# Optimization experiments

Measured on AMD Instinct MI355X. Metric: run time of the kernel, lower is better.

The kernel has to match this reference:

```python
import jax, jax.numpy as jnp
import numpy as np

# Model dims
B, S, H, E, I, K = 2, 2048, 1024, 8, 1024, 2
ALPHA, LIMIT = 1.702, 7.0  # gpt_oss activation constants (module defaults)


def setup_inputs() -> dict:
    key = jax.random.key(0)
    ks = jax.random.split(key, 5)
    sc = 0.02
    return {
        "hidden_states": jax.random.normal(ks[0], (B, S, H), jnp.float32),
        "router_weight": jax.random.normal(ks[1], (H, E), jnp.float32) * sc,
        "gate_up_proj": jax.random.normal(ks[2], (E, H, 2 * I), jnp.float32) * sc,
        "gate_up_proj_bias": jnp.zeros((E, 2 * I), jnp.float32),
        "down_proj": jax.random.normal(ks[3], (E, I, H), jnp.float32) * sc,
        "down_proj_bias": jnp.zeros((E, H), jnp.float32),
    }


def reference(hidden_states, router_weight, gate_up_proj, gate_up_proj_bias,
              down_proj, down_proj_bias):
    Bt, St, Ht = hidden_states.shape
    x = hidden_states.reshape(-1, Ht)           # [T, H], T = B*S
    T = x.shape[0]

    # Router: linear -> top-k -> softmax over selected logits (gpt_oss style)
    logits = x @ router_weight                  # [T, E]
    top_vals, top_idx = jax.lax.top_k(logits, K)
    scores = jax.nn.softmax(top_vals, axis=-1)  # [T, K]
    # Sparse combine weights: w[t, e] = score if e selected for t, else 0
    w = jnp.zeros((T, E), x.dtype).at[jnp.arange(T)[:, None], top_idx].set(scores)

    # Fused gate+up projection for every expert (dense equivalent of grouped GEMM;
    # unselected experts get zero combine weight so math matches sparse path)
    gu = jnp.einsum('th,ehf->tef', x, gate_up_proj) + gate_up_proj_bias  # [T, E, 2I]
    gate = gu[..., ::2]                         # interleaved gate (default)
    up = gu[..., 1::2]
    gate = jnp.minimum(gate, LIMIT)
    up = jnp.clip(up, -LIMIT, LIMIT)
    glu = gate * jax.nn.sigmoid(gate * ALPHA)
    act = (up + 1.0) * glu                      # [T, E, I]

    down = jnp.einsum('tei,eih->teh', act, down_proj) + down_proj_bias  # [T, E, H]

    # Weighted combine over experts (all-to-all combine is identity at D=1)
    out = jnp.einsum('te,teh->th', w, down)     # [T, H]
    return out.reshape(Bt, St, Ht)
```

## Files before the change

### kernel.cpp

```cpp
#include <hip/hip_runtime.h>
#include <hip/hip_bf16.h>
#include <cstdint>
#include <cstddef>

constexpr int T_TOK = 4096;
constexpr int H_DIM = 1024;
constexpr int E_NUM = 8;
constexpr int I_DIM = 1024;
constexpr int F2    = 2048;
constexpr float ALPHA = 1.702f;
constexpr float LIMIT = 7.0f;
constexpr int BM = 128;
constexpr int BK = 64;
constexpr int NKT = 16;
constexpr int MAXT = 72;

using u16    = unsigned short;
using bf16x8 = __attribute__((ext_vector_type(8))) __bf16;
using s16x8  = __attribute__((ext_vector_type(8))) short;
using f32x4  = __attribute__((ext_vector_type(4))) float;

constexpr size_t WS_W1T  = 0;
constexpr size_t WS_DOWN = 0;
constexpr size_t WS_W2T  = 33554432;
constexpr size_t WS_ACT  = 50331648;
constexpr size_t WS_ETOK = 67108864;
constexpr size_t WS_POS  = 67239936;
constexpr size_t WS_CNT  = 67272704;
constexpr size_t WS_ROWB = 67272736;
constexpr size_t WS_ASGN = 67272768;
constexpr size_t WS_TOPE = 67273792;
constexpr size_t WS_TOPW = 67290176;
constexpr size_t WS_XBF  = 67322944;
constexpr size_t WS_NEED = 75711552;

__device__ __forceinline__ u16 f2bf(float f) {
    union { float f; unsigned u; } v; v.f = f;
    return (u16)((v.u + 0x7FFFu + ((v.u >> 16) & 1u)) >> 16);
}
__device__ __forceinline__ float bf2f(u16 u) {
    union { unsigned u; float f; } v; v.u = (unsigned)u << 16; return v.f;
}

__device__ __forceinline__ s16x8 pack8(float4 a, float4 b) {
    s16x8 r;
    r[0] = (short)f2bf(a.x); r[1] = (short)f2bf(a.y);
    r[2] = (short)f2bf(a.z); r[3] = (short)f2bf(a.w);
    r[4] = (short)f2bf(b.x); r[5] = (short)f2bf(b.y);
    r[6] = (short)f2bf(b.z); r[7] = (short)f2bf(b.w);
    return r;
}

__device__ __forceinline__ void gload16(const void* g, void* l) {
    __builtin_amdgcn_global_load_lds((const __attribute__((address_space(1))) unsigned*)g,
                                     (__attribute__((address_space(3))) unsigned*)l,
                                     16, 0, 0);
}

__device__ __forceinline__ void pipe_sync() {
    __builtin_amdgcn_sched_barrier(0);
    asm volatile("s_waitcnt vmcnt(0) lgkmcnt(0)" ::: "memory");
    __builtin_amdgcn_s_barrier();
    __builtin_amdgcn_sched_barrier(0);
}

__global__ __launch_bounds__(256) void k_xbf(const float* __restrict__ x,
                                             u16* __restrict__ xbf) {
    const size_t i = ((size_t)blockIdx.x * 256 + threadIdx.x) * 8;
    float4 a = *(const float4*)(x + i);
    float4 b = *(const float4*)(x + i + 4);
    *(s16x8*)(xbf + i) = pack8(a, b);
}

__global__ __launch_bounds__(256) void k_transpose_w1(const float* __restrict__ in,
                                                      u16* __restrict__ out) {
    __shared__ float tile[64][65];
    const int e = blockIdx.z, c0 = blockIdx.x * 64, h0 = blockIdx.y * 64;
    const int tid = threadIdx.x;
    const float* src = in + ((size_t)e * H_DIM + h0) * F2 + c0;
#pragma unroll
    for (int i = 0; i < 4; ++i) {
        int r = (tid >> 4) + i * 16, c = (tid & 15) * 4;
        float4 v = *(const float4*)(src + (size_t)r * F2 + c);
        tile[r][c] = v.x; tile[r][c + 1] = v.y; tile[r][c + 2] = v.z; tile[r][c + 3] = v.w;
    }
    __syncthreads();
    const int c = tid >> 2, hseg = (tid & 3) * 16;
    const int g = c & 1;
    const int f = (c0 + c) >> 1;
    u16* dst = out + (((size_t)e * 2 + g) * I_DIM + f) * H_DIM + h0 + hseg;
    s16x8 o0, o1;
#pragma unroll
    for (int j = 0; j < 8; ++j) o0[j] = (short)f2bf(tile[hseg + j][c]);
#pragma unroll
    for (int j = 0; j < 8; ++j) o1[j] = (short)f2bf(tile[hseg + 8 + j][c]);
    *(s16x8*)dst = o0;
    *(s16x8*)(dst + 8) = o1;
}

__global__ __launch_bounds__(256) void k_transpose_w2(const float* __restrict__ in,
                                                      u16* __restrict__ out) {
    __shared__ float tile[64][65];
    const int e = blockIdx.z, h0 = blockIdx.x * 64, i0 = blockIdx.y * 64;
    const int tid = threadIdx.x;
    const float* src = in + ((size_t)e * I_DIM + i0) * H_DIM + h0;
#pragma unroll
    for (int i = 0; i < 4; ++i) {
        int r = (tid >> 4) + i * 16, c = (tid & 15) * 4;
        float4 v = *(const float4*)(src + (size_t)r * H_DIM + c);
        tile[r][c] = v.x; tile[r][c + 1] = v.y; tile[r][c + 2] = v.z; tile[r][c + 3] = v.w;
    }
    __syncthreads();
    const int c = tid >> 2, iseg = (tid & 3) * 16;
    u16* dst = out + ((size_t)e * H_DIM + h0 + c) * I_DIM + i0 + iseg;
    s16x8 o0, o1;
#pragma unroll
    for (int j = 0; j < 8; ++j) o0[j] = (short)f2bf(tile[iseg + j][c]);
#pragma unroll
    for (int j = 0; j < 8; ++j) o1[j] = (short)f2bf(tile[iseg + 8 + j][c]);
    *(s16x8*)dst = o0;
    *(s16x8*)(dst + 8) = o1;
}

__global__ __launch_bounds__(256) void k_router_top2(const float* __restrict__ x,
                                                     const float* __restrict__ rw,
                                                     int* __restrict__ tope,
                                                     float2* __restrict__ topw) {
    const int wave = threadIdx.x >> 6, lane = threadIdx.x & 63;
    const int t = blockIdx.x * 4 + wave;
    const float* xr = x + (size_t)t * H_DIM;
    float acc[E_NUM];
#pragma unroll
    for (int e = 0; e < E_NUM; ++e) acc[e] = 0.f;
    for (int h = lane; h < H_DIM; h += 64) {
        float xv = xr[h];
        const float* r = rw + h * E_NUM;
#pragma unroll
        for (int e = 0; e < E_NUM; ++e) acc[e] += xv * r[e];
    }
#pragma unroll
    for (int e = 0; e < E_NUM; ++e) {
        float v = acc[e];
#pragma unroll
        for (int o = 32; o > 0; o >>= 1) v += __shfl_down(v, o);
        acc[e] = v;
    }
    if (lane == 0) {
        int e0 = 0; float v0 = acc[0];
#pragma unroll
        for (int e = 1; e < E_NUM; ++e) if (acc[e] > v0) { v0 = acc[e]; e0 = e; }
        int e1 = -1; float v1 = -3.4e38f;
#pragma unroll
        for (int e = 0; e < E_NUM; ++e) if (e != e0 && acc[e] > v1) { v1 = acc[e]; e1 = e; }
        float ew = expf(v1 - v0);
        float inv = 1.f / (1.f + ew);
        tope[t] = e0 | (e1 << 8);
        topw[t] = make_float2(inv, ew * inv);
    }
}

__global__ __launch_bounds__(256) void k_router_scatter(const int* __restrict__ tope,
                                                        int* __restrict__ cnt,
                                                        int* __restrict__ ent_tok,
                                                        int2* __restrict__ pos) {
    __shared__ int lcnt[E_NUM];
    __shared__ int gbase[E_NUM];
    const int tid = threadIdx.x;
    const int t = blockIdx.x * 256 + tid;
    if (tid < E_NUM) lcnt[tid] = 0;
    __syncthreads();
    const int pk = tope[t];
    const int e0 = pk & 0xff, e1 = pk >> 8;
    const int o0 = atomicAdd(&lcnt[e0], 1);
    const int o1 = atomicAdd(&lcnt[e1], 1);
    __syncthreads();
    if (tid < E_NUM) gbase[tid] = atomicAdd(&cnt[tid], lcnt[tid]);
    __syncthreads();
    const int p0 = gbase[e0] + o0;
    const int p1 = gbase[e1] + o1;
    ent_tok[e0 * T_TOK + p0] = t;
    ent_tok[e1 * T_TOK + p1] = t;
    pos[t] = make_int2(p0, p1);
}

__global__ void k_schedule(const int* __restrict__ cnt, int* __restrict__ rowbase,
                           int* __restrict__ assign) {
    if (threadIdx.x == 0) {
        int rb = 0, na = 0;
        for (int e = 0; e < E_NUM; ++e) {
            rowbase[e] = rb;
            int nt = (cnt[e] + BM - 1) >> 7;
            for (int m = 0; m < nt; ++m) assign[na++] = (e << 16) | m;
            rb += cnt[e];
        }
        for (; na < MAXT; ++na) assign[na] = -1;
    }
}

__global__ __launch_bounds__(256, 2) void k_gemm1(
    const u16* __restrict__ xbf, const u16* __restrict__ w1t,
    const float* __restrict__ bias, const int* __restrict__ ent_tok,
    const int* __restrict__ cnt, const int* __restrict__ rowbase,
    const int* __restrict__ assign, u16* __restrict__ act) {
    const int a = assign[blockIdx.y];
    if (a < 0) return;
    const int e = a >> 16, mt = a & 0xffff;
    const int j0 = blockIdx.x * 64;
    const int cs = cnt[e], r0 = mt * BM;
    __shared__ __align__(16) u16 As[2][BM * BK];
    __shared__ __align__(16) u16 Bs[2][BM * BK];
    const int tid = threadIdx.x, lane = tid & 63, wv = tid >> 6;
    const int lr8 = lane >> 3;
    const int sg  = (lane & 7) ^ lr8;
    const u16* asrc[4]; const u16* bsrc[4]; int dofs[4];
#pragma unroll
    for (int j = 0; j < 4; ++j) {
        const int row = j * 32 + wv * 8 + lr8;
        const int aent = r0 + row;
        const int tok = (aent < cs) ? ent_tok[e * T_TOK + aent] : 0;
        asrc[j] = xbf + (size_t)tok * H_DIM + sg * 8;
        const int g = row >> 6;
        const int f = j0 + (row & 63);
        bsrc[j] = w1t + (((size_t)e * 2 + g) * I_DIM + f) * H_DIM + sg * 8;
        dofs[j] = (j * 32 + wv * 8) * BK;
    }
    const int wm = wv >> 1, wn = wv & 1;
    const int lcol = lane & 15, lk = lane >> 4;
    int aoff[4][2], goff[2][2], uoff[2][2];
#pragma unroll
    for (int mi = 0; mi < 4; ++mi) {
        const int r = wm * 64 + mi * 16 + lcol;
#pragma unroll
        for (int h = 0; h < 2; ++h)
            aoff[mi][h] = r * 128 + (((h * 4 + lk) ^ (r & 7)) << 4);
    }
#pragma unroll
    for (int nj = 0; nj < 2; ++nj) {
        const int rg_ = wn * 32 + nj * 16 + lcol;
        const int ru  = 64 + rg_;
#pragma unroll
        for (int h = 0; h < 2; ++h) {
            goff[nj][h] = rg_ * 128 + (((h * 4 + lk) ^ (rg_ & 7)) << 4);
            uoff[nj][h] = ru  * 128 + (((h * 4 + lk) ^ (ru  & 7)) << 4);
        }
    }
    f32x4 ag[4][2], au[4][2];
    const f32x4 z = {0.f, 0.f, 0.f, 0.f};
#pragma unroll
    for (int mi = 0; mi < 4; ++mi) { ag[mi][0] = z; ag[mi][1] = z; au[mi][0] = z; au[mi][1] = z; }
#pragma unroll
    for (int j = 0; j < 4; ++j) {
        gload16(asrc[j], &As[0][dofs[j]]);
        gload16(bsrc[j], &Bs[0][dofs[j]]);
    }
    pipe_sync();
    int cur = 0;
    for (int t = 0; t < NKT; ++t) {
        if (t + 1 < NKT) {
            const int kn = (t + 1) * BK;
            u16* Ad = As[cur ^ 1]; u16* Bd = Bs[cur ^ 1];
#pragma unroll
            for (int j = 0; j < 4; ++j) {
                gload16(asrc[j] + kn, Ad + dofs[j]);
                gload16(bsrc[j] + kn, Bd + dofs[j]);
            }
        }
        const char* Ab = (const char*)(&As[cur][0]);
        const char* Bb = (const char*)(&Bs[cur][0]);
#pragma unroll
        for (int h = 0; h < 2; ++h) {
            bf16x8 af[4];
#pragma unroll
            for (int mi = 0; mi < 4; ++mi) af[mi] = *(const bf16x8*)(Ab + aoff[mi][h]);
            const bf16x8 g0 = *(const bf16x8*)(Bb + goff[0][h]);
            const bf16x8 g1 = *(const bf16x8*)(Bb + goff[1][h]);
            const bf16x8 u0 = *(const bf16x8*)(Bb + uoff[0][h]);
            const bf16x8 u1 = *(const bf16x8*)(Bb + uoff[1][h]);
            __builtin_amdgcn_s_setprio(1);
#pragma unroll
            for (int mi = 0; mi < 4; ++mi) {
                ag[mi][0] = __builtin_amdgcn_mfma_f32_16x16x32_bf16(af[mi], g0, ag[mi][0], 0, 0, 0);
                au[mi][0] = __builtin_amdgcn_mfma_f32_16x16x32_bf16(af[mi], u0, au[mi][0], 0, 0, 0);
                ag[mi][1] = __builtin_amdgcn_mfma_f32_16x16x32_bf16(af[mi], g1, ag[mi][1], 0, 0, 0);
                au[mi][1] = __builtin_amdgcn_mfma_f32_16x16x32_bf16(af[mi], u1, au[mi][1], 0, 0, 0);
            }
            __builtin_amdgcn_s_setprio(0);
        }
        pipe_sync();
        cur ^= 1;
    }
    const int rbase = rowbase[e];
#pragma unroll
    for (int mi = 0; mi < 4; ++mi) {
#pragma unroll
        for (int nj = 0; nj < 2; ++nj) {
            const int col = j0 + wn * 32 + nj * 16 + lcol;
            const float bg_ = bias[e * F2 + 2 * col];
            const float bu_ = bias[e * F2 + 2 * col + 1];
#pragma unroll
            for (int rg = 0; rg < 4; ++rg) {
                const int r = wm * 64 + mi * 16 + lk * 4 + rg;
                if (r0 + r < cs) {
                    float gv = ag[mi][nj][rg] + bg_;
                    float uv = au[mi][nj][rg] + bu_;
                    gv = fminf(gv, LIMIT);
                    uv = fminf(fmaxf(uv, -LIMIT), LIMIT);
                    const float glu = gv / (1.f + expf(-ALPHA * gv));
                    act[(size_t)(rbase + r0 + r) * I_DIM + col] = f2bf((uv + 1.f) * glu);
                }
            }
        }
    }
}

__global__ __launch_bounds__(256, 2) void k_gemm2(
    const u16* __restrict__ act, const u16* __restrict__ w2t,
    const int* __restrict__ cnt, const int* __restrict__ rowbase,
    const int* __restrict__ assign, u16* __restrict__ down) {
    const int a = assign[blockIdx.y];
    if (a < 0) return;
    const int e = a >> 16, mt = a & 0xffff;
    const int n0 = blockIdx.x * 128;
    const int cs = cnt[e], r0 = mt * BM, rbase = rowbase[e];
    __shared__ __align__(16) u16 As[2][BM * BK];
    __shared__ __align__(16) u16 Bs[2][BM * BK];
    const int tid = threadIdx.x, lane = tid & 63, wv = tid >> 6;
    const int lr8 = lane >> 3;
    const int sg  = (lane & 7) ^ lr8;
    const u16* asrc[4]; const u16* bsrc[4]; int dofs[4];
#pragma unroll
    for (int j = 0; j < 4; ++j) {
        const int row = j * 32 + wv * 8 + lr8;
        int ar = rbase + r0 + row;
        if (ar > 2 * T_TOK - 1) ar = 2 * T_TOK - 1;
        asrc[j] = act + (size_t)ar * I_DIM + sg * 8;
        bsrc[j] = w2t + ((size_t)e * H_DIM + n0 + row) * I_DIM + sg * 8;
        dofs[j] = (j * 32 + wv * 8) * BK;
    }
    const int wm = wv >> 1, wn = wv & 1;
    const int lcol = lane & 15, lk = lane >> 4;
    int aoff[4][2], boff[4][2];
#pragma unroll
    for (int mi = 0; mi < 4; ++mi) {
        const int r = wm * 64 + mi * 16 + lcol;
        const int b = wn * 64 + mi * 16 + lcol;
#pragma unroll
        for (int h = 0; h < 2; ++h) {
            aoff[mi][h] = r * 128 + (((h * 4 + lk) ^ (r & 7)) << 4);
            boff[mi][h] = b * 128 + (((h * 4 + lk) ^ (b & 7)) << 4);
        }
    }
    f32x4 acc[4][4];
    const f32x4 z = {0.f, 0.f, 0.f, 0.f};
#pragma unroll
    for (int mi = 0; mi < 4; ++mi)
#pragma unroll
        for (int nj = 0; nj < 4; ++nj) acc[mi][nj] = z;
#pragma unroll
    for (int j = 0; j < 4; ++j) {
        gload16(asrc[j], &As[0][dofs[j]]);
        gload16(bsrc[j], &Bs[0][dofs[j]]);
    }
    pipe_sync();
    int cur = 0;
    for (int t = 0; t < NKT; ++t) {
        if (t + 1 < NKT) {
            const int kn = (t + 1) * BK;
            u16* Ad = As[cur ^ 1]; u16* Bd = Bs[cur ^ 1];
#pragma unroll
            for (int j = 0; j < 4; ++j) {
                gload16(asrc[j] + kn, Ad + dofs[j]);
                gload16(bsrc[j] + kn, Bd + dofs[j]);
            }
        }
        const char* Ab = (const char*)(&As[cur][0]);
        const char* Bb = (const char*)(&Bs[cur][0]);
#pragma unroll
        for (int h = 0; h < 2; ++h) {
            bf16x8 af[4], bf_[4];
#pragma unroll
            for (int mi = 0; mi < 4; ++mi) af[mi]  = *(const bf16x8*)(Ab + aoff[mi][h]);
#pragma unroll
            for (int nj = 0; nj < 4; ++nj) bf_[nj] = *(const bf16x8*)(Bb + boff[nj][h]);
            __builtin_amdgcn_s_setprio(1);
#pragma unroll
            for (int mi = 0; mi < 4; ++mi)
#pragma unroll
                for (int nj = 0; nj < 4; ++nj)
                    acc[mi][nj] = __builtin_amdgcn_mfma_f32_16x16x32_bf16(af[mi], bf_[nj], acc[mi][nj], 0, 0, 0);
            __builtin_amdgcn_s_setprio(0);
        }
        pipe_sync();
        cur ^= 1;
    }
#pragma unroll
    for (int mi = 0; mi < 4; ++mi) {
#pragma unroll
        for (int nj = 0; nj < 4; ++nj) {
            const int col = n0 + wn * 64 + nj * 16 + lcol;
#pragma unroll
            for (int rg = 0; rg < 4; ++rg) {
                const int r = wm * 64 + mi * 16 + lk * 4 + rg;
                if (r0 + r < cs)
                    down[(size_t)(rbase + r0 + r) * H_DIM + col] = f2bf(acc[mi][nj][rg]);
            }
        }
    }
}

__global__ __launch_bounds__(256) void k_combine(
    const int* __restrict__ tope, const float2* __restrict__ topw,
    const int2* __restrict__ pos, const int* __restrict__ rowb,
    const float* __restrict__ b2, const u16* __restrict__ down,
    float* __restrict__ out) {
    const int t = blockIdx.x;
    const int c = threadIdx.x * 4;
    const int pk = tope[t];
    const int e0 = pk & 0xff, e1 = pk >> 8;
    const int2 pp = pos[t];
    const float2 w = topw[t];
    const size_t ro0 = (size_t)(rowb[e0] + pp.x) * H_DIM;
    const size_t ro1 = (size_t)(rowb[e1] + pp.y) * H_DIM;
    ushort4 d0 = *(const ushort4*)(down + ro0 + c);
    ushort4 d1 = *(const ushort4*)(down + ro1 + c);
    float4 bb0 = *(const float4*)(b2 + e0 * H_DIM + c);
    float4 bb1 = *(const float4*)(b2 + e1 * H_DIM + c);
    float4 o;
    o.x = w.x * (bf2f(d0.x) + bb0.x) + w.y * (bf2f(d1.x) + bb1.x);
    o.y = w.x * (bf2f(d0.y) + bb0.y) + w.y * (bf2f(d1.y) + bb1.y);
    o.z = w.x * (bf2f(d0.z) + bb0.z) + w.y * (bf2f(d1.z) + bb1.z);
    o.w = w.x * (bf2f(d0.w) + bb0.w) + w.y * (bf2f(d1.w) + bb1.w);
    *(float4*)(out + (size_t)t * H_DIM + c) = o;
}

extern "C" void kernel_launch(void* const* d_in, const int* in_sizes, int n_in,
                              void* d_out, int out_size, void* d_ws, size_t ws_size,
                              hipStream_t stream) {
    const float* x   = (const float*)d_in[0];
    const float* rw  = (const float*)d_in[1];
    const float* w1  = (const float*)d_in[2];
    const float* b1  = (const float*)d_in[3];
    const float* w2  = (const float*)d_in[4];
    const float* b2  = (const float*)d_in[5];
    float* out = (float*)d_out;
    char* ws = (char*)d_ws;

    if (ws_size < WS_NEED) return;

    u16*    W1T  = (u16*)(ws + WS_W1T);
    u16*    DOWN = (u16*)(ws + WS_DOWN);
    u16*    W2T  = (u16*)(ws + WS_W2T);
    u16*    ACT  = (u16*)(ws + WS_ACT);
    int*    ETOK = (int*)(ws + WS_ETOK);
    int2*   POS  = (int2*)(ws + WS_POS);
    int*    CNT  = (int*)(ws + WS_CNT);
    int*    ROWB = (int*)(ws + WS_ROWB);
    int*    ASGN = (int*)(ws + WS_ASGN);
    int*    TOPE = (int*)(ws + WS_TOPE);
    float2* TOPW = (float2*)(ws + WS_TOPW);
    u16*    XBF  = (u16*)(ws + WS_XBF);

    hipMemsetAsync(CNT, 0, E_NUM * sizeof(int), stream);

    k_xbf<<<T_TOK * H_DIM / 2048, 256, 0, stream>>>(x, XBF);
    k_transpose_w1<<<dim3(32, 16, 8), 256, 0, stream>>>(w1, W1T);
    k_transpose_w2<<<dim3(16, 16, 8), 256, 0, stream>>>(w2, W2T);
    k_router_top2<<<T_TOK / 4, 256, 0, stream>>>(x, rw, TOPE, TOPW);
    k_router_scatter<<<T_TOK / 256, 256, 0, stream>>>(TOPE, CNT, ETOK, POS);
    k_schedule<<<1, 64, 0, stream>>>(CNT, ROWB, ASGN);
    k_gemm1<<<dim3(16, MAXT), 256, 0, stream>>>(XBF, W1T, b1, ETOK, CNT, ROWB, ASGN, ACT);
    k_gemm2<<<dim3(8, MAXT), 256, 0, stream>>>(ACT, W2T, CNT, ROWB, ASGN, DOWN);
    k_combine<<<T_TOK, 256, 0, stream>>>(TOPE, TOPW, POS, ROWB, b2, DOWN, out);
}
```

Baseline: 179.4 us.

## Rework expert GEMMs into 512-thread blocks with quarter-staged pipelined loads

Both grouped GEMM kernels move to 8-wave blocks with larger tiles: gemm1 covers 128 tokens by 128 activation columns, and gemm2 covers 256 rows by 128 columns with its own tile schedule. The K loop is split into four sub-phases, each issuing part of the next tile's global-to-LDS loads with a partial vmcnt wait before its MFMAs, replacing the single full drain per tile. The aim is better overlap of memory and compute, more operand reuse per block and fewer blocks. The cost is more barriers per iteration, hand-tuned wait counts that must match the load order exactly, and a larger LDS footprint that may cut occupancy.

```diff
diff --git a/kernel.cpp b/kernel.cpp
--- a/kernel.cpp
+++ b/kernel.cpp
@@ -10,10 +10,10 @@
 constexpr int F2    = 2048;
 constexpr float ALPHA = 1.702f;
 constexpr float LIMIT = 7.0f;
-constexpr int BM = 128;
-constexpr int BK = 64;
+constexpr int BK  = 64;
 constexpr int NKT = 16;
-constexpr int MAXT = 72;
+constexpr int MAXT1 = 72;
+constexpr int MAXT2 = 40;
 
 using u16    = unsigned short;
 using bf16x8 = __attribute__((ext_vector_type(8))) __bf16;
@@ -28,7 +28,8 @@
 constexpr size_t WS_POS  = 67239936;
 constexpr size_t WS_CNT  = 67272704;
 constexpr size_t WS_ROWB = 67272736;
-constexpr size_t WS_ASGN = 67272768;
+constexpr size_t WS_ASG1 = 67272768;
+constexpr size_t WS_ASG2 = 67272768 + 512;
 constexpr size_t WS_TOPE = 67273792;
 constexpr size_t WS_TOPW = 67290176;
 constexpr size_t WS_XBF  = 67322944;
@@ -57,12 +58,8 @@
                                      16, 0, 0);
 }
 
-__device__ __forceinline__ void pipe_sync() {
-    __builtin_amdgcn_sched_barrier(0);
-    asm volatile("s_waitcnt vmcnt(0) lgkmcnt(0)" ::: "memory");
-    __builtin_amdgcn_s_barrier();
-    __builtin_amdgcn_sched_barrier(0);
-}
+#define BAR() __builtin_amdgcn_s_barrier()
+#define WVM(n) asm volatile("s_waitcnt vmcnt(" #n ")" ::: "memory")
 
 __global__ __launch_bounds__(256) void k_xbf(const float* __restrict__ x,
                                              u16* __restrict__ xbf) {
@@ -184,20 +181,23 @@
 }
 
 __global__ void k_schedule(const int* __restrict__ cnt, int* __restrict__ rowbase,
-                           int* __restrict__ assign) {
+                           int* __restrict__ a1, int* __restrict__ a2) {
     if (threadIdx.x == 0) {
-        int rb = 0, na = 0;
+        int rb = 0, n1 = 0, n2 = 0;
         for (int e = 0; e < E_NUM; ++e) {
             rowbase[e] = rb;
-            int nt = (cnt[e] + BM - 1) >> 7;
-            for (int m = 0; m < nt; ++m) assign[na++] = (e << 16) | m;
+            int t1 = (cnt[e] + 127) >> 7;
+            for (int m = 0; m < t1; ++m) a1[n1++] = (e << 16) | m;
+            int t2 = (cnt[e] + 255) >> 8;
+            for (int m = 0; m < t2; ++m) a2[n2++] = (e << 16) | m;
             rb += cnt[e];
         }
-        for (; na < MAXT; ++na) assign[na] = -1;
-    }
-}
-
-__global__ __launch_bounds__(256, 2) void k_gemm1(
+        for (; n1 < MAXT1; ++n1) a1[n1] = -1;
+        for (; n2 < MAXT2; ++n2) a2[n2] = -1;
+    }
+}
+
+__global__ __launch_bounds__(512, 2) void k_gemm1(
     const u16* __restrict__ xbf, const u16* __restrict__ w1t,
     const float* __restrict__ bias, const int* __restrict__ ent_tok,
     const int* __restrict__ cnt, const int* __restrict__ rowbase,
@@ -205,207 +205,348 @@
     const int a = assign[blockIdx.y];
     if (a < 0) return;
     const int e = a >> 16, mt = a & 0xffff;
-    const int j0 = blockIdx.x * 64;
-    const int cs = cnt[e], r0 = mt * BM;
-    __shared__ __align__(16) u16 As[2][BM * BK];
-    __shared__ __align__(16) u16 Bs[2][BM * BK];
+    const int j0 = blockIdx.x * 128;
+    const int cs = cnt[e], r0 = mt * 128, rbase = rowbase[e];
+    __shared__ __align__(16) u16 As[2 * 2 * 64 * 64];
+    __shared__ __align__(16) u16 Bs[2 * 2 * 128 * 64];
     const int tid = threadIdx.x, lane = tid & 63, wv = tid >> 6;
+    const int lcol = lane & 15, lk = lane >> 4;
     const int lr8 = lane >> 3;
-    const int sg  = (lane & 7) ^ lr8;
-    const u16* asrc[4]; const u16* bsrc[4]; int dofs[4];
-#pragma unroll
-    for (int j = 0; j < 4; ++j) {
-        const int row = j * 32 + wv * 8 + lr8;
-        const int aent = r0 + row;
-        const int tok = (aent < cs) ? ent_tok[e * T_TOK + aent] : 0;
-        asrc[j] = xbf + (size_t)tok * H_DIM + sg * 8;
-        const int g = row >> 6;
-        const int f = j0 + (row & 63);
-        bsrc[j] = w1t + (((size_t)e * 2 + g) * I_DIM + f) * H_DIM + sg * 8;
-        dofs[j] = (j * 32 + wv * 8) * BK;
-    }
-    const int wm = wv >> 1, wn = wv & 1;
-    const int lcol = lane & 15, lk = lane >> 4;
-    int aoff[4][2], goff[2][2], uoff[2][2];
-#pragma unroll
-    for (int mi = 0; mi < 4; ++mi) {
-        const int r = wm * 64 + mi * 16 + lcol;
-#pragma unroll
-        for (int h = 0; h < 2; ++h)
-            aoff[mi][h] = r * 128 + (((h * 4 + lk) ^ (r & 7)) << 4);
-    }
-#pragma unroll
-    for (int nj = 0; nj < 2; ++nj) {
-        const int rg_ = wn * 32 + nj * 16 + lcol;
-        const int ru  = 64 + rg_;
-#pragma unroll
-        for (int h = 0; h < 2; ++h) {
-            goff[nj][h] = rg_ * 128 + (((h * 4 + lk) ^ (rg_ & 7)) << 4);
-            uoff[nj][h] = ru  * 128 + (((h * 4 + lk) ^ (ru  & 7)) << 4);
+    const int sg  = (lane & 7) ^ (lr8 & 7);
+
+    const int arow0 = 0 * 64 + wv * 8 + lr8;
+    const int arow1 = 1 * 64 + wv * 8 + lr8;
+    const int ae0 = r0 + arow0, ae1 = r0 + arow1;
+    const int tok0 = (ae0 < cs) ? ent_tok[e * T_TOK + ae0] : 0;
+    const int tok1 = (ae1 < cs) ? ent_tok[e * T_TOK + ae1] : 0;
+    const u16* aS0 = xbf + (size_t)tok0 * H_DIM + sg * 8;
+    const u16* aS1 = xbf + (size_t)tok1 * H_DIM + sg * 8;
+    const u16* bS[2][2];
+#pragma unroll
+    for (int h = 0; h < 2; ++h)
+#pragma unroll
+        for (int i = 0; i < 2; ++i) {
+            const int brow = h * 128 + i * 64 + wv * 8 + lr8;
+            const int pair = brow >> 4, gu = pair & 1;
+            const int acol = j0 + (pair >> 1) * 16 + (brow & 15);
+            bS[h][i] = w1t + (((size_t)e * 2 + gu) * I_DIM + acol) * H_DIM + sg * 8;
         }
-    }
-    f32x4 ag[4][2], au[4][2];
+
+    int swz[2];
+#pragma unroll
+    for (int kk = 0; kk < 2; ++kk) swz[kk] = (((kk * 4 + lk) ^ (lcol & 7)) << 4);
+    int aro[2], bro[2];
+#pragma unroll
+    for (int mi = 0; mi < 2; ++mi) aro[mi] = ((wv & 1) * 32 + mi * 16 + lcol) * 128;
+#pragma unroll
+    for (int nj = 0; nj < 2; ++nj) bro[nj] = ((wv >> 1) * 32 + nj * 16 + lcol) * 128;
+    const char* AbC = (const char*)As;
+    const char* BbC = (const char*)Bs;
+
+    f32x4 acc[2][2][2][2];
     const f32x4 z = {0.f, 0.f, 0.f, 0.f};
 #pragma unroll
-    for (int mi = 0; mi < 4; ++mi) { ag[mi][0] = z; ag[mi][1] = z; au[mi][0] = z; au[mi][1] = z; }
-#pragma unroll
-    for (int j = 0; j < 4; ++j) {
-        gload16(asrc[j], &As[0][dofs[j]]);
-        gload16(bsrc[j], &Bs[0][dofs[j]]);
-    }
-    pipe_sync();
-    int cur = 0;
-    for (int t = 0; t < NKT; ++t) {
-        if (t + 1 < NKT) {
-            const int kn = (t + 1) * BK;
-            u16* Ad = As[cur ^ 1]; u16* Bd = Bs[cur ^ 1];
-#pragma unroll
-            for (int j = 0; j < 4; ++j) {
-                gload16(asrc[j] + kn, Ad + dofs[j]);
-                gload16(bsrc[j] + kn, Bd + dofs[j]);
-            }
-        }
-        const char* Ab = (const char*)(&As[cur][0]);
-        const char* Bb = (const char*)(&Bs[cur][0]);
-#pragma unroll
-        for (int h = 0; h < 2; ++h) {
-            bf16x8 af[4];
-#pragma unroll
-            for (int mi = 0; mi < 4; ++mi) af[mi] = *(const bf16x8*)(Ab + aoff[mi][h]);
-            const bf16x8 g0 = *(const bf16x8*)(Bb + goff[0][h]);
-            const bf16x8 g1 = *(const bf16x8*)(Bb + goff[1][h]);
-            const bf16x8 u0 = *(const bf16x8*)(Bb + uoff[0][h]);
-            const bf16x8 u1 = *(const bf16x8*)(Bb + uoff[1][h]);
-            __builtin_amdgcn_s_setprio(1);
-#pragma unroll
-            for (int mi = 0; mi < 4; ++mi) {
-                ag[mi][0] = __builtin_amdgcn_mfma_f32_16x16x32_bf16(af[mi], g0, ag[mi][0], 0, 0, 0);
-                au[mi][0] = __builtin_amdgcn_mfma_f32_16x16x32_bf16(af[mi], u0, au[mi][0], 0, 0, 0);
-                ag[mi][1] = __builtin_amdgcn_mfma_f32_16x16x32_bf16(af[mi], g1, ag[mi][1], 0, 0, 0);
-                au[mi][1] = __builtin_amdgcn_mfma_f32_16x16x32_bf16(af[mi], u1, au[mi][1], 0, 0, 0);
-            }
-            __builtin_amdgcn_s_setprio(0);
-        }
-        pipe_sync();
-        cur ^= 1;
-    }
-    const int rbase = rowbase[e];
-#pragma unroll
-    for (int mi = 0; mi < 4; ++mi) {
-#pragma unroll
-        for (int nj = 0; nj < 2; ++nj) {
-            const int col = j0 + wn * 32 + nj * 16 + lcol;
-            const float bg_ = bias[e * F2 + 2 * col];
-            const float bu_ = bias[e * F2 + 2 * col + 1];
-#pragma unroll
-            for (int rg = 0; rg < 4; ++rg) {
-                const int r = wm * 64 + mi * 16 + lk * 4 + rg;
-                if (r0 + r < cs) {
-                    float gv = ag[mi][nj][rg] + bg_;
-                    float uv = au[mi][nj][rg] + bu_;
-                    gv = fminf(gv, LIMIT);
-                    uv = fminf(fmaxf(uv, -LIMIT), LIMIT);
-                    const float glu = gv / (1.f + expf(-ALPHA * gv));
-                    act[(size_t)(rbase + r0 + r) * I_DIM + col] = f2bf((uv + 1.f) * glu);
+    for (int mh = 0; mh < 2; ++mh)
+#pragma unroll
+        for (int mi = 0; mi < 2; ++mi)
+#pragma unroll
+            for (int nh = 0; nh < 2; ++nh)
+#pragma unroll
+                for (int nj = 0; nj < 2; ++nj) acc[mh][mi][nh][nj] = z;
+
+    gload16(aS0, (u16*)As + 0 * 4096 + wv * 512);
+    gload16(aS1, (u16*)As + 1 * 4096 + wv * 512);
+    gload16(bS[0][0], (u16*)Bs + 0 * 8192 + 0 * 4096 + wv * 512);
+    gload16(bS[0][1], (u16*)Bs + 0 * 8192 + 1 * 4096 + wv * 512);
+    gload16(bS[1][0], (u16*)Bs + 1 * 8192 + 0 * 4096 + wv * 512);
+    gload16(bS[1][1], (u16*)Bs + 1 * 8192 + 1 * 4096 + wv * 512);
+    WVM(0);
+    BAR();
+
+    bf16x8 aF[2][2], bF0[2][2], bF1[2][2];
+
+    for (int kt = 0; kt < NKT; ++kt) {
+        const int d = kt & 1, d2 = d ^ 1;
+        const int dA = d * 16384, dB = d * 32768;
+        const int kno = (kt + 1) * BK;
+        const bool st = (kt + 1 < NKT);
+
+        if (st) { gload16(aS0 + kno, (u16*)As + (d2 * 2 + 0) * 4096 + wv * 512); WVM(4); }
+        else    { WVM(3); }
+        BAR();
+#pragma unroll
+        for (int mi = 0; mi < 2; ++mi)
+#pragma unroll
+            for (int kk = 0; kk < 2; ++kk)
+                aF[mi][kk] = *(const bf16x8*)(AbC + dA + 0 * 8192 + aro[mi] + swz[kk]);
+#pragma unroll
+        for (int nj = 0; nj < 2; ++nj)
+#pragma unroll
+            for (int kk = 0; kk < 2; ++kk)
+                bF0[nj][kk] = *(const bf16x8*)(BbC + dB + 0 * 16384 + bro[nj] + swz[kk]);
+        __builtin_amdgcn_s_setprio(1);
+#pragma unroll
+        for (int mi = 0; mi < 2; ++mi)
+#pragma unroll
+            for (int nj = 0; nj < 2; ++nj)
+#pragma unroll
+                for (int kk = 0; kk < 2; ++kk)
+                    acc[0][mi][0][nj] = __builtin_amdgcn_mfma_f32_16x16x32_bf16(aF[mi][kk], bF0[nj][kk], acc[0][mi][0][nj], 0, 0, 0);
+        __builtin_amdgcn_s_setprio(0);
+        BAR();
+
+        if (st) {
+            gload16(bS[0][0] + kno, (u16*)Bs + (d2 * 2 + 0) * 8192 + 0 * 4096 + wv * 512);
+            gload16(bS[0][1] + kno, (u16*)Bs + (d2 * 2 + 0) * 8192 + 1 * 4096 + wv * 512);
+            WVM(4);
+        } else { WVM(1); }
+        BAR();
+#pragma unroll
+        for (int nj = 0; nj < 2; ++nj)
+#pragma unroll
+            for (int kk = 0; kk < 2; ++kk)
+                bF1[nj][kk] = *(const bf16x8*)(BbC + dB + 1 * 16384 + bro[nj] + swz[kk]);
+        __builtin_amdgcn_s_setprio(1);
+#pragma unroll
+        for (int mi = 0; mi < 2; ++mi)
+#pragma unroll
+            for (int nj = 0; nj < 2; ++nj)
+#pragma unroll
+                for (int kk = 0; kk < 2; ++kk)
+                    acc[0][mi][1][nj] = __builtin_amdgcn_mfma_f32_16x16x32_bf16(aF[mi][kk], bF1[nj][kk], acc[0][mi][1][nj], 0, 0, 0);
+        __builtin_amdgcn_s_setprio(0);
+        BAR();
+
+        if (st) {
+            gload16(bS[1][0] + kno, (u16*)Bs + (d2 * 2 + 1) * 8192 + 0 * 4096 + wv * 512);
+            gload16(bS[1][1] + kno, (u16*)Bs + (d2 * 2 + 1) * 8192 + 1 * 4096 + wv * 512);
+            WVM(5);
+        } else { WVM(0); }
+        BAR();
+#pragma unroll
+        for (int mi = 0; mi < 2; ++mi)
+#pragma unroll
+            for (int kk = 0; kk < 2; ++kk)
+                aF[mi][kk] = *(const bf16x8*)(AbC + dA + 1 * 8192 + aro[mi] + swz[kk]);
+        __builtin_amdgcn_s_setprio(1);
+#pragma unroll
+        for (int mi = 0; mi < 2; ++mi)
+#pragma unroll
+            for (int nj = 0; nj < 2; ++nj)
+#pragma unroll
+                for (int kk = 0; kk < 2; ++kk)
+                    acc[1][mi][0][nj] = __builtin_amdgcn_mfma_f32_16x16x32_bf16(aF[mi][kk], bF0[nj][kk], acc[1][mi][0][nj], 0, 0, 0);
+        __builtin_amdgcn_s_setprio(0);
+        BAR();
+
+        if (st) gload16(aS1 + kno, (u16*)As + (d2 * 2 + 1) * 4096 + wv * 512);
+        BAR();
+        __builtin_amdgcn_s_setprio(1);
+#pragma unroll
+        for (int mi = 0; mi < 2; ++mi)
+#pragma unroll
+            for (int nj = 0; nj < 2; ++nj)
+#pragma unroll
+                for (int kk = 0; kk < 2; ++kk)
+                    acc[1][mi][1][nj] = __builtin_amdgcn_mfma_f32_16x16x32_bf16(aF[mi][kk], bF1[nj][kk], acc[1][mi][1][nj], 0, 0, 0);
+        __builtin_amdgcn_s_setprio(0);
+        BAR();
+    }
+
+#pragma unroll
+    for (int mh = 0; mh < 2; ++mh)
+#pragma unroll
+        for (int mi = 0; mi < 2; ++mi)
+#pragma unroll
+            for (int nh = 0; nh < 2; ++nh) {
+                const int acol = j0 + (nh * 4 + (wv >> 1)) * 16 + lcol;
+                const float bg_ = bias[e * F2 + 2 * acol];
+                const float bu_ = bias[e * F2 + 2 * acol + 1];
+#pragma unroll
+                for (int rg = 0; rg < 4; ++rg) {
+                    const int row = mh * 64 + (wv & 1) * 32 + mi * 16 + lk * 4 + rg;
+                    if (r0 + row < cs) {
+                        float gv = acc[mh][mi][nh][0][rg] + bg_;
+                        float uv = acc[mh][mi][nh][1][rg] + bu_;
+                        gv = fminf(gv, LIMIT);
+                        uv = fminf(fmaxf(uv, -LIMIT), LIMIT);
+                        const float glu = gv / (1.f + expf(-ALPHA * gv));
+                        act[(size_t)(rbase + r0 + row) * I_DIM + acol] = f2bf((uv + 1.f) * glu);
+                    }
                 }
             }
-        }
-    }
-}
-
-__global__ __launch_bounds__(256, 2) void k_gemm2(
-    const u16* __restrict__ act, const u16* __restrict__ w2t,
+}
+
+__global__ __launch_bounds__(512, 2) void k_gemm2(
+    const u16* __restrict__ actb, const u16* __restrict__ w2t,
     const int* __restrict__ cnt, const int* __restrict__ rowbase,
     const int* __restrict__ assign, u16* __restrict__ down) {
     const int a = assign[blockIdx.y];
     if (a < 0) return;
     const int e = a >> 16, mt = a & 0xffff;
     const int n0 = blockIdx.x * 128;
-    const int cs = cnt[e], r0 = mt * BM, rbase = rowbase[e];
-    __shared__ __align__(16) u16 As[2][BM * BK];
-    __shared__ __align__(16) u16 Bs[2][BM * BK];
+    const int cs = cnt[e], r0 = mt * 256, rbase = rowbase[e];
+    __shared__ __align__(16) u16 As[2 * 2 * 128 * 64];
+    __shared__ __align__(16) u16 Bs[2 * 2 * 64 * 64];
     const int tid = threadIdx.x, lane = tid & 63, wv = tid >> 6;
+    const int lcol = lane & 15, lk = lane >> 4;
     const int lr8 = lane >> 3;
-    const int sg  = (lane & 7) ^ lr8;
-    const u16* asrc[4]; const u16* bsrc[4]; int dofs[4];
-#pragma unroll
-    for (int j = 0; j < 4; ++j) {
-        const int row = j * 32 + wv * 8 + lr8;
-        int ar = rbase + r0 + row;
-        if (ar > 2 * T_TOK - 1) ar = 2 * T_TOK - 1;
-        asrc[j] = act + (size_t)ar * I_DIM + sg * 8;
-        bsrc[j] = w2t + ((size_t)e * H_DIM + n0 + row) * I_DIM + sg * 8;
-        dofs[j] = (j * 32 + wv * 8) * BK;
-    }
-    const int wm = wv >> 1, wn = wv & 1;
-    const int lcol = lane & 15, lk = lane >> 4;
-    int aoff[4][2], boff[4][2];
-#pragma unroll
-    for (int mi = 0; mi < 4; ++mi) {
-        const int r = wm * 64 + mi * 16 + lcol;
-        const int b = wn * 64 + mi * 16 + lcol;
-#pragma unroll
-        for (int h = 0; h < 2; ++h) {
-            aoff[mi][h] = r * 128 + (((h * 4 + lk) ^ (r & 7)) << 4);
-            boff[mi][h] = b * 128 + (((h * 4 + lk) ^ (b & 7)) << 4);
+    const int sg  = (lane & 7) ^ (lr8 & 7);
+
+    const u16* aS[2][2];
+#pragma unroll
+    for (int h = 0; h < 2; ++h)
+#pragma unroll
+        for (int i = 0; i < 2; ++i) {
+            const int row = h * 128 + i * 64 + wv * 8 + lr8;
+            int ar = rbase + r0 + row;
+            if (ar > 2 * T_TOK - 1) ar = 2 * T_TOK - 1;
+            aS[h][i] = actb + (size_t)ar * I_DIM + sg * 8;
         }
-    }
-    f32x4 acc[4][4];
+    const u16* bS[2];
+#pragma unroll
+    for (int h = 0; h < 2; ++h) {
+        const int brow = h * 64 + wv * 8 + lr8;
+        bS[h] = w2t + ((size_t)e * H_DIM + n0 + brow) * I_DIM + sg * 8;
+    }
+
+    int swz[2];
+#pragma unroll
+    for (int kk = 0; kk < 2; ++kk) swz[kk] = (((kk * 4 + lk) ^ (lcol & 7)) << 4);
+    int aro[2], bro[2];
+#pragma unroll
+    for (int mi = 0; mi < 2; ++mi) aro[mi] = ((wv & 3) * 32 + mi * 16 + lcol) * 128;
+#pragma unroll
+    for (int nj = 0; nj < 2; ++nj) bro[nj] = ((wv >> 2) * 32 + nj * 16 + lcol) * 128;
+    const char* AbC = (const char*)As;
+    const char* BbC = (const char*)Bs;
+
+    f32x4 acc[2][2][2][2];
     const f32x4 z = {0.f, 0.f, 0.f, 0.f};
 #pragma unroll
-    for (int mi = 0; mi < 4; ++mi)
-#pragma unroll
-        for (int nj = 0; nj < 4; ++nj) acc[mi][nj] = z;
-#pragma unroll
-    for (int j = 0; j < 4; ++j) {
-        gload16(asrc[j], &As[0][dofs[j]]);
-        gload16(bsrc[j], &Bs[0][dofs[j]]);
-    }
-    pipe_sync();
-    int cur = 0;
-    for (int t = 0; t < NKT; ++t) {
-        if (t + 1 < NKT) {
-            const int kn = (t + 1) * BK;
-            u16* Ad = As[cur ^ 1]; u16* Bd = Bs[cur ^ 1];
-#pragma unroll
-            for (int j = 0; j < 4; ++j) {
-                gload16(asrc[j] + kn, Ad + dofs[j]);
-                gload16(bsrc[j] + kn, Bd + dofs[j]);
-            }
+    for (int mh = 0; mh < 2; ++mh)
+#pragma unroll
+        for (int mi = 0; mi < 2; ++mi)
+#pragma unroll
+            for (int nh = 0; nh < 2; ++nh)
+#pragma unroll
+                for (int nj = 0; nj < 2; ++nj) acc[mh][mi][nh][nj] = z;
+
+    gload16(aS[0][0], (u16*)As + 0 * 8192 + 0 * 4096 + wv * 512);
+    gload16(aS[0][1], (u16*)As + 0 * 8192 + 1 * 4096 + wv * 512);
+    gload16(bS[0],    (u16*)Bs + 0 * 4096 + wv * 512);
+    gload16(bS[1],    (u16*)Bs + 1 * 4096 + wv * 512);
+    gload16(aS[1][0], (u16*)As + 1 * 8192 + 0 * 4096 + wv * 512);
+    gload16(aS[1][1], (u16*)As + 1 * 8192 + 1 * 4096 + wv * 512);
+    WVM(0);
+    BAR();
+
+    bf16x8 aF[2][2], bF0[2][2], bF1[2][2];
+
+    for (int kt = 0; kt < NKT; ++kt) {
+        const int d = kt & 1, d2 = d ^ 1;
+        const int dA = d * 32768, dB = d * 16384;
+        const int kno = (kt + 1) * BK;
+        const bool st = (kt + 1 < NKT);
+
+        if (st) {
+            gload16(aS[0][0] + kno, (u16*)As + (d2 * 2 + 0) * 8192 + 0 * 4096 + wv * 512);
+            gload16(aS[0][1] + kno, (u16*)As + (d2 * 2 + 0) * 8192 + 1 * 4096 + wv * 512);
+            WVM(5);
+        } else { WVM(3); }
+        BAR();
+#pragma unroll
+        for (int mi = 0; mi < 2; ++mi)
+#pragma unroll
+            for (int kk = 0; kk < 2; ++kk)
+                aF[mi][kk] = *(const bf16x8*)(AbC + dA + 0 * 16384 + aro[mi] + swz[kk]);
+#pragma unroll
+        for (int nj = 0; nj < 2; ++nj)
+#pragma unroll
+            for (int kk = 0; kk < 2; ++kk)
+                bF0[nj][kk] = *(const bf16x8*)(BbC + dB + 0 * 8192 + bro[nj] + swz[kk]);
+        __builtin_amdgcn_s_setprio(1);
+#pragma unroll
+        for (int mi = 0; mi < 2; ++mi)
+#pragma unroll
+            for (int nj = 0; nj < 2; ++nj)
+#pragma unroll
+                for (int kk = 0; kk < 2; ++kk)
+                    acc[0][mi][0][nj] = __builtin_amdgcn_mfma_f32_16x16x32_bf16(aF[mi][kk], bF0[nj][kk], acc[0][mi][0][nj], 0, 0, 0);
+        __builtin_amdgcn_s_setprio(0);
+        BAR();
+
+        if (st) { gload16(bS[0] + kno, (u16*)Bs + (d2 * 2 + 0) * 4096 + wv * 512); WVM(5); }
+        else    { WVM(2); }
+        BAR();
+#pragma unroll
+        for (int nj = 0; nj < 2; ++nj)
+#pragma unroll
+            for (int kk = 0; kk < 2; ++kk)
+                bF1[nj][kk] = *(const bf16x8*)(BbC + dB + 1 * 8192 + bro[nj] + swz[kk]);
+        __builtin_amdgcn_s_setprio(1);
+#pragma unroll
+        for (int mi = 0; mi < 2; ++mi)
+#pragma unroll
+            for (int nj = 0; nj < 2; ++nj)
+#pragma unroll
+                for (int kk = 0; kk < 2; ++kk)
+                    acc[0][mi][1][nj] = __builtin_amdgcn_mfma_f32_16x16x32_bf16(aF[mi][kk], bF1[nj][kk], acc[0][mi][1][nj], 0, 0, 0);
+        __builtin_amdgcn_s_setprio(0);
+        BAR();
+
+        if (st) { gload16(bS[1] + kno, (u16*)Bs + (d2 * 2 + 1) * 4096 + wv * 512); WVM(4); }
+        else    { WVM(0); }
+        BAR();
+#pragma unroll
+        for (int mi = 0; mi < 2; ++mi)
+#pragma unroll
+            for (int kk = 0; kk < 2; ++kk)
+                aF[mi][kk] = *(const bf16x8*)(AbC + dA + 1 * 16384 + aro[mi] + swz[kk]);
+        __builtin_amdgcn_s_setprio(1);
+#pragma unroll
+        for (int mi = 0; mi < 2; ++mi)
+#pragma unroll
+            for (int nj = 0; nj < 2; ++nj)
+#pragma unroll
+                for (int kk = 0; kk < 2; ++kk)
+                    acc[1][mi][0][nj] = __builtin_amdgcn_mfma_f32_16x16x32_bf16(aF[mi][kk], bF0[nj][kk], acc[1][mi][0][nj], 0, 0, 0);
+        __builtin_amdgcn_s_setprio(0);
+        BAR();
+
+        if (st) {
+            gload16(aS[1][0] + kno, (u16*)As + (d2 * 2 + 1) * 8192 + 0 * 4096 + wv * 512);
+            gload16(aS[1][1] + kno, (u16*)As + (d2 * 2 + 1) * 8192 + 1 * 4096 + wv * 512);
         }
-        const char* Ab = (const char*)(&As[cur][0]);
-        const char* Bb = (const char*)(&Bs[cur][0]);
-#pragma unroll
-        for (int h = 0; h < 2; ++h) {
-            bf16x8 af[4], bf_[4];
-#pragma unroll
-            for (int mi = 0; mi < 4; ++mi) af[mi]  = *(const bf16x8*)(Ab + aoff[mi][h]);
-#pragma unroll
-            for (int nj = 0; nj < 4; ++nj) bf_[nj] = *(const bf16x8*)(Bb + boff[nj][h]);
-            __builtin_amdgcn_s_setprio(1);
-#pragma unroll
-            for (int mi = 0; mi < 4; ++mi)
-#pragma unroll
-                for (int nj = 0; nj < 4; ++nj)
-                    acc[mi][nj] = __builtin_amdgcn_mfma_f32_16x16x32_bf16(af[mi], bf_[nj], acc[mi][nj], 0, 0, 0);
-            __builtin_amdgcn_s_setprio(0);
-        }
-        pipe_sync();
-        cur ^= 1;
-    }
-#pragma unroll
-    for (int mi = 0; mi < 4; ++mi) {
-#pragma unroll
-        for (int nj = 0; nj < 4; ++nj) {
-            const int col = n0 + wn * 64 + nj * 16 + lcol;
-#pragma unroll
-            for (int rg = 0; rg < 4; ++rg) {
-                const int r = wm * 64 + mi * 16 + lk * 4 + rg;
-                if (r0 + r < cs)
-                    down[(size_t)(rbase + r0 + r) * H_DIM + col] = f2bf(acc[mi][nj][rg]);
-            }
-        }
-    }
+        BAR();
+        __builtin_amdgcn_s_setprio(1);
+#pragma unroll
+        for (int mi = 0; mi < 2; ++mi)
+#pragma unroll
+            for (int nj = 0; nj < 2; ++nj)
+#pragma unroll
+                for (int kk = 0; kk < 2; ++kk)
+                    acc[1][mi][1][nj] = __builtin_amdgcn_mfma_f32_16x16x32_bf16(aF[mi][kk], bF1[nj][kk], acc[1][mi][1][nj], 0, 0, 0);
+        __builtin_amdgcn_s_setprio(0);
+        BAR();
+    }
+
+#pragma unroll
+    for (int mh = 0; mh < 2; ++mh)
+#pragma unroll
+        for (int mi = 0; mi < 2; ++mi)
+#pragma unroll
+            for (int nh = 0; nh < 2; ++nh)
+#pragma unroll
+                for (int nj = 0; nj < 2; ++nj) {
+                    const int col = n0 + nh * 64 + (wv >> 2) * 32 + nj * 16 + lcol;
+#pragma unroll
+                    for (int rg = 0; rg < 4; ++rg) {
+                        const int row = mh * 128 + (wv & 3) * 32 + mi * 16 + lk * 4 + rg;
+                        if (r0 + row < cs)
+                            down[(size_t)(rbase + r0 + row) * H_DIM + col] = f2bf(acc[mh][mi][nh][nj][rg]);
+                    }
+                }
 }
 
 __global__ __launch_bounds__(256) void k_combine(
@@ -455,7 +596,8 @@
     int2*   POS  = (int2*)(ws + WS_POS);
     int*    CNT  = (int*)(ws + WS_CNT);
     int*    ROWB = (int*)(ws + WS_ROWB);
-    int*    ASGN = (int*)(ws + WS_ASGN);
+    int*    ASG1 = (int*)(ws + WS_ASG1);
+    int*    ASG2 = (int*)(ws + WS_ASG2);
     int*    TOPE = (int*)(ws + WS_TOPE);
     float2* TOPW = (float2*)(ws + WS_TOPW);
     u16*    XBF  = (u16*)(ws + WS_XBF);
@@ -467,8 +609,8 @@
     k_transpose_w2<<<dim3(16, 16, 8), 256, 0, stream>>>(w2, W2T);
     k_router_top2<<<T_TOK / 4, 256, 0, stream>>>(x, rw, TOPE, TOPW);
     k_router_scatter<<<T_TOK / 256, 256, 0, stream>>>(TOPE, CNT, ETOK, POS);
-    k_schedule<<<1, 64, 0, stream>>>(CNT, ROWB, ASGN);
-    k_gemm1<<<dim3(16, MAXT), 256, 0, stream>>>(XBF, W1T, b1, ETOK, CNT, ROWB, ASGN, ACT);
-    k_gemm2<<<dim3(8, MAXT), 256, 0, stream>>>(ACT, W2T, CNT, ROWB, ASGN, DOWN);
+    k_schedule<<<1, 64, 0, stream>>>(CNT, ROWB, ASG1, ASG2);
+    k_gemm1<<<dim3(8, MAXT1), 512, 0, stream>>>(XBF, W1T, b1, ETOK, CNT, ROWB, ASG1, ACT);
+    k_gemm2<<<dim3(8, MAXT2), 512, 0, stream>>>(ACT, W2T, CNT, ROWB, ASG2, DOWN);
     k_combine<<<T_TOK, 256, 0, stream>>>(TOPE, TOPW, POS, ROWB, b2, DOWN, out);
 }
```

Result: slower. 197.7 us (+10.2%).
